# Performance work log

Hardware: AMD Instinct MI355X
Metric: run time of the kernel (lower is better)

Reference implementation:

```python
import jax, jax.numpy as jnp
import numpy as np

B, S, H = 2, 2048, 2048
NH, KVH, HD = 16, 4, 128
R = 16
LORA_SCALE = 32.0 / 16.0  # lora_alpha / lora_r
ATTN_SCALE = HD ** -0.5
NEG = -1e9


def setup_inputs() -> dict:
    key = jax.random.key(0)
    ks = jax.random.split(key, 16)
    q_dim, kv_dim = NH * HD, KVH * HD
    # RoPE tables
    inv_freq = 1.0 / (10000.0 ** (jnp.arange(0, HD, 2, dtype=jnp.float32) / HD))
    ang = jnp.arange(S, dtype=jnp.float32)[:, None] * inv_freq[None, :]  # [S, HD/2]
    emb = jnp.concatenate([ang, ang], axis=-1)  # [S, HD]
    cos = jnp.broadcast_to(jnp.cos(emb)[None], (B, S, HD))
    sin = jnp.broadcast_to(jnp.sin(emb)[None], (B, S, HD))
    # additive causal mask [B,1,S,S]
    causal = jnp.triu(jnp.full((S, S), NEG, dtype=jnp.float32), k=1)
    attention_mask = jnp.broadcast_to(causal[None, None], (B, 1, S, S))
    return {
        'hidden_states': jax.random.normal(ks[0], (B, S, H), jnp.float32),
        'cos': cos,
        'sin': sin,
        'attention_mask': attention_mask,
        'q_w': jax.random.normal(ks[1], (q_dim, H), jnp.float32) * 0.02,
        'k_w': jax.random.normal(ks[2], (kv_dim, H), jnp.float32) * 0.02,
        'v_w': jax.random.normal(ks[3], (kv_dim, H), jnp.float32) * 0.02,
        'q_b': jax.random.normal(ks[4], (q_dim,), jnp.float32) * 0.02,
        'k_b': jax.random.normal(ks[5], (kv_dim,), jnp.float32) * 0.02,
        'v_b': jax.random.normal(ks[6], (kv_dim,), jnp.float32) * 0.02,
        'q_A': jax.random.normal(ks[7], (H, R), jnp.float32) * (1.0 / np.sqrt(H)),
        'q_B': jax.random.normal(ks[8], (R, q_dim), jnp.float32) * 0.02,
        'k_A': jax.random.normal(ks[9], (H, R), jnp.float32) * (1.0 / np.sqrt(H)),
        'k_B': jax.random.normal(ks[10], (R, kv_dim), jnp.float32) * 0.02,
        'v_A': jax.random.normal(ks[11], (H, R), jnp.float32) * (1.0 / np.sqrt(H)),
        'v_B': jax.random.normal(ks[12], (R, kv_dim), jnp.float32) * 0.02,
        'o_w': jax.random.normal(ks[13], (H, H), jnp.float32) * 0.02,
    }


def _rotate_half(x):
    x1, x2 = x[..., : HD // 2], x[..., HD // 2:]
    return jnp.concatenate([-x2, x1], axis=-1)


def reference(hidden_states, cos, sin, attention_mask,
              q_w, k_w, v_w, q_b, k_b, v_b,
              q_A, q_B, k_A, k_B, v_A, v_B, o_w):
    x = hidden_states  # dropout p=0 (eval)
    # fused base + LoRA projections
    q = x @ q_w.T + q_b + LORA_SCALE * ((x @ q_A) @ q_B)  # [B,S,NH*HD]
    k = x @ k_w.T + k_b + LORA_SCALE * ((x @ k_A) @ k_B)  # [B,S,KVH*HD]
    v = x @ v_w.T + v_b + LORA_SCALE * ((x @ v_A) @ v_B)
    q = q.reshape(B, S, NH, HD).transpose(0, 2, 1, 3)   # [B,NH,S,HD]
    k = k.reshape(B, S, KVH, HD).transpose(0, 2, 1, 3)  # [B,KVH,S,HD]
    v = v.reshape(B, S, KVH, HD).transpose(0, 2, 1, 3)
    # RoPE
    c = cos[:, None]  # [B,1,S,HD]
    s = sin[:, None]
    q = q * c + _rotate_half(q) * s
    k = k * c + _rotate_half(k) * s
    # GQA: repeat kv heads
    n_rep = NH // KVH
    k = jnp.repeat(k, n_rep, axis=1)  # [B,NH,S,HD]
    v = jnp.repeat(v, n_rep, axis=1)
    scores = jnp.einsum('bhqd,bhkd->bhqk', q, k) * ATTN_SCALE
    scores = scores + attention_mask
    attn = jax.nn.softmax(scores.astype(jnp.float32), axis=-1).astype(q.dtype)
    out = jnp.einsum('bhqk,bhkd->bhqd', attn, v)
    out = out.transpose(0, 2, 1, 3).reshape(B, S, NH * HD)  # [B,S,H]
    return out @ o_w.T
```

## Files before the change

kernel.cpp:

```cpp
#include <hip/hip_runtime.h>

constexpr int cB   = 2;
constexpr int cS   = 2048;
constexpr int cH   = 2048;
constexpr int cNH  = 16;
constexpr int cKVH = 4;
constexpr int cHD  = 128;
constexpr int cQD  = 2048;
constexpr int cKVD = 512;
constexpr int cNQKV = 3072;
constexpr int cNTOK = 4096;
#define ATTN_SCALE 0.08838834764831845f
#define QSCALE 0.12751589549581288f

typedef __bf16 bf16;
typedef __attribute__((ext_vector_type(8))) __bf16 bf16x8;
typedef __attribute__((ext_vector_type(4))) __bf16 bf16x4;
typedef __attribute__((ext_vector_type(4))) float  f32x4;

__device__ __forceinline__ void async_load16(const bf16* g, bf16* l) {
    __builtin_amdgcn_global_load_lds(
        (const __attribute__((address_space(1))) void*)g,
        (__attribute__((address_space(3))) void*)l, 16, 0, 0);
}

__global__ void conv_f32_bf16(const float* __restrict__ in, bf16* __restrict__ out) {
    int i = (blockIdx.x * 256 + threadIdx.x) * 4;
    f32x4 v = *(const f32x4*)(in + i);
    bf16x4 o;
    o[0] = (bf16)v[0]; o[1] = (bf16)v[1]; o[2] = (bf16)v[2]; o[3] = (bf16)v[3];
    *(bf16x4*)(out + i) = o;
}

__global__ __launch_bounds__(256) void prep_w2(
        const float* __restrict__ qw, const float* __restrict__ kw, const float* __restrict__ vw,
        const float* __restrict__ qA, const float* __restrict__ qB,
        const float* __restrict__ kA, const float* __restrict__ kB,
        const float* __restrict__ vA, const float* __restrict__ vB,
        const float* __restrict__ qb, const float* __restrict__ kbias, const float* __restrict__ vb,
        bf16* __restrict__ Wc, float* __restrict__ biasc) {
    const int wave = threadIdx.x >> 6, lane = threadIdx.x & 63;
    const int n = blockIdx.y * 4 + wave;
    const int k0 = blockIdx.x * 512 + lane * 8;
    const float* W; const float* Am; const float* Bm; const float* bias; int nn, nd;
    if (n < cQD)             { W = qw; Am = qA; Bm = qB; bias = qb;    nn = n;               nd = cQD; }
    else if (n < cQD + cKVD) { W = kw; Am = kA; Bm = kB; bias = kbias; nn = n - cQD;         nd = cKVD; }
    else                     { W = vw; Am = vA; Bm = vB; bias = vb;    nn = n - cQD - cKVD;  nd = cKVD; }
    if (blockIdx.x == 0 && lane == 0) biasc[n] = bias[nn];
    float bm[16];
    #pragma unroll
    for (int r = 0; r < 16; ++r) bm[r] = Bm[r * nd + nn];
    const float* wrow = W + (size_t)nn * cH + k0;
    f32x4 w0 = *(const f32x4*)(wrow);
    f32x4 w1 = *(const f32x4*)(wrow + 4);
    bf16x8 o;
    #pragma unroll
    for (int j = 0; j < 8; ++j) {
        const f32x4* am = (const f32x4*)(Am + (size_t)(k0 + j) * 16);
        f32x4 a0 = am[0], a1 = am[1], a2 = am[2], a3 = am[3];
        float acc = 0.f;
        #pragma unroll
        for (int c = 0; c < 4; ++c) acc += a0[c] * bm[c] + a1[c] * bm[4 + c]
                                         + a2[c] * bm[8 + c] + a3[c] * bm[12 + c];
        const float wv = (j < 4) ? w0[j] : w1[j - 4];
        o[j] = (bf16)(wv + 2.0f * acc);
    }
    *(bf16x8*)&Wc[(size_t)n * cH + k0] = o;
}

__global__ __launch_bounds__(256) void gemm_qkv(const bf16* __restrict__ A, const bf16* __restrict__ Bw,
                                                const float* __restrict__ bias,
                                                const float* __restrict__ cosb, const float* __restrict__ sinb,
                                                bf16* __restrict__ Qr, bf16* __restrict__ Kr,
                                                bf16* __restrict__ Vt) {
    __shared__ bf16 Al[128 * 64];
    __shared__ bf16 Bl[128 * 64];
    const int tid = threadIdx.x;
    const int wave = tid >> 6, lane = tid & 63;
    const int quad = lane >> 4, l16 = lane & 15;
    const int wr = wave >> 1, wc = wave & 1;
    const long bm = (long)blockIdx.y * 128, bn = (long)blockIdx.x * 128;
    const int K = cH;

    f32x4 acc[4][4];
    #pragma unroll
    for (int i = 0; i < 4; ++i)
        #pragma unroll
        for (int c = 0; c < 4; ++c) acc[i][c] = f32x4{0.f, 0.f, 0.f, 0.f};

    int ago[4], slo[4];
    #pragma unroll
    for (int i2 = 0; i2 < 4; ++i2) {
        const int si = i2 * 256 + tid;
        const int row = si >> 3, c8 = si & 7;
        const int csw = c8 ^ (row & 7);
        ago[i2] = row * K + csw * 8;
        slo[i2] = si * 8;
    }
    const size_t bmK = (size_t)bm * K, bnK = (size_t)bn * K;
    const int sw = l16 & 7;

    for (int k0 = 0; k0 < K; k0 += 64) {
        __syncthreads();
        #pragma unroll
        for (int i2 = 0; i2 < 4; ++i2) async_load16(A  + bmK + k0 + ago[i2], Al + slo[i2]);
        #pragma unroll
        for (int i2 = 0; i2 < 4; ++i2) async_load16(Bw + bnK + k0 + ago[i2], Bl + slo[i2]);
        __syncthreads();
        #pragma unroll
        for (int ks = 0; ks < 2; ++ks) {
            const int g = ks * 4 + quad;
            const int cofs = (g ^ sw) * 8;
            bf16x8 af[4], bfr[4];
            #pragma unroll
            for (int i = 0; i < 4; ++i)
                af[i] = *(const bf16x8*)&Al[(wr * 64 + i * 16 + l16) * 64 + cofs];
            #pragma unroll
            for (int c = 0; c < 4; ++c) {
                const int nrow = wc * 32 + (c & 1) * 16 + (c >> 1) * 64 + l16;
                bfr[c] = *(const bf16x8*)&Bl[nrow * 64 + cofs];
            }
            #pragma unroll
            for (int i = 0; i < 4; ++i)
                #pragma unroll
                for (int c = 0; c < 4; ++c)
                    acc[i][c] = __builtin_amdgcn_mfma_f32_16x16x32_bf16(af[i], bfr[c], acc[i][c], 0, 0, 0);
        }
    }

    #pragma unroll
    for (int c = 0; c < 4; ++c) {
        const int nloc = wc * 32 + (c & 1) * 16 + (c >> 1) * 64 + l16;
        const float bv = bias[bn + nloc];
        #pragma unroll
        for (int i = 0; i < 4; ++i)
            #pragma unroll
            for (int r = 0; r < 4; ++r) acc[i][c][r] += bv;
    }

    const int head = (int)(bn >> 7);
    if (head < cNH + cKVH) {
        const bool isQ = head < cNH;
        #pragma unroll
        for (int cl = 0; cl < 2; ++cl) {
            const int d = wc * 32 + cl * 16 + l16;
            #pragma unroll
            for (int i = 0; i < 4; ++i)
                #pragma unroll
                for (int r = 0; r < 4; ++r) {
                    const long t = bm + wr * 64 + i * 16 + quad * 4 + r;
                    const float cv = cosb[t * cHD + d];
                    const float sv = sinb[t * cHD + d];
                    const float v1 = acc[i][cl][r], v2 = acc[i][cl + 2][r];
                    float o1 = v1 * cv - v2 * sv;
                    float o2 = v2 * cv + v1 * sv;
                    if (isQ) { o1 *= QSCALE; o2 *= QSCALE; }
                    const int b = (int)(t >> 11), s = (int)(t & 2047);
                    bf16* dst = isQ
                        ? Qr + ((size_t)(b * cNH + head) * cS + s) * cHD
                        : Kr + ((size_t)(b * cKVH + (head - cNH)) * cS + s) * cHD;
                    dst[d]      = (bf16)o1;
                    dst[d + 64] = (bf16)o2;
                }
        }
    } else {
        const int kv = head - cNH - cKVH;
        const int b = (int)(bm >> 11);
        const int sbase = (int)(bm & 2047);
        #pragma unroll
        for (int c = 0; c < 4; ++c) {
            const int d = wc * 32 + (c & 1) * 16 + (c >> 1) * 64 + l16;
            #pragma unroll
            for (int i = 0; i < 4; ++i) {
                const int s0 = sbase + wr * 64 + i * 16 + quad * 4;
                bf16x4 o4;
                #pragma unroll
                for (int r = 0; r < 4; ++r) o4[r] = (bf16)acc[i][c][r];
                *(bf16x4*)&Vt[((size_t)((b * cKVH + kv) * cHD) + d) * cS + s0] = o4;
            }
        }
    }
}

__global__ __launch_bounds__(256) void gemm_bt_f32(const bf16* __restrict__ A, const bf16* __restrict__ Bw,
                                                   float* __restrict__ Cp, int M, int N, int K) {
    __shared__ bf16 Al[128 * 64];
    __shared__ bf16 Bl[128 * 64];
    const int tid = threadIdx.x;
    const int wave = tid >> 6, lane = tid & 63;
    const int quad = lane >> 4, l16 = lane & 15;
    const int wr = wave >> 1, wc = wave & 1;
    const long bm = (long)blockIdx.y * 128, bn = (long)blockIdx.x * 128;

    f32x4 acc[4][4];
    #pragma unroll
    for (int i = 0; i < 4; ++i)
        #pragma unroll
        for (int c = 0; c < 4; ++c) acc[i][c] = f32x4{0.f, 0.f, 0.f, 0.f};

    int ago[4], slo[4];
    #pragma unroll
    for (int i2 = 0; i2 < 4; ++i2) {
        const int si = i2 * 256 + tid;
        const int row = si >> 3, c8 = si & 7;
        const int csw = c8 ^ (row & 7);
        ago[i2] = row * K + csw * 8;
        slo[i2] = si * 8;
    }
    const size_t bmK = (size_t)bm * K, bnK = (size_t)bn * K;
    const int sw = l16 & 7;

    for (int k0 = 0; k0 < K; k0 += 64) {
        __syncthreads();
        #pragma unroll
        for (int i2 = 0; i2 < 4; ++i2) async_load16(A  + bmK + k0 + ago[i2], Al + slo[i2]);
        #pragma unroll
        for (int i2 = 0; i2 < 4; ++i2) async_load16(Bw + bnK + k0 + ago[i2], Bl + slo[i2]);
        __syncthreads();
        #pragma unroll
        for (int ks = 0; ks < 2; ++ks) {
            const int cofs = ((ks * 4 + quad) ^ sw) * 8;
            bf16x8 af[4], bfr[4];
            #pragma unroll
            for (int i = 0; i < 4; ++i)
                af[i] = *(const bf16x8*)&Al[(wr * 64 + i * 16 + l16) * 64 + cofs];
            #pragma unroll
            for (int c = 0; c < 4; ++c)
                bfr[c] = *(const bf16x8*)&Bl[(wc * 64 + c * 16 + l16) * 64 + cofs];
            #pragma unroll
            for (int i = 0; i < 4; ++i)
                #pragma unroll
                for (int c = 0; c < 4; ++c)
                    acc[i][c] = __builtin_amdgcn_mfma_f32_16x16x32_bf16(af[i], bfr[c], acc[i][c], 0, 0, 0);
        }
    }

    #pragma unroll
    for (int i = 0; i < 4; ++i)
        #pragma unroll
        for (int c = 0; c < 4; ++c) {
            const long m0 = bm + wr * 64 + i * 16 + quad * 4;
            const long n  = bn + wc * 64 + c * 16 + l16;
            #pragma unroll
            for (int r = 0; r < 4; ++r)
                Cp[(m0 + r) * N + n] = acc[i][c][r];
        }
}

__global__ __launch_bounds__(256, 2) void flash4(const bf16* __restrict__ Q, const bf16* __restrict__ K,
                                                 const bf16* __restrict__ Vt, bf16* __restrict__ Ob) {
    __shared__ bf16 kb[8192];
    __shared__ bf16 vb[8192];
    __shared__ bf16 pb[4096];
    const int tid = threadIdx.x;
    const int wave = tid >> 6, lane = tid & 63;
    const int quad = lane >> 4, l16 = lane & 15;
    const int pi = blockIdx.x;
    const int h = blockIdx.y, b = blockIdx.z;

    const bf16* Qh = Q  + (size_t)(b * cNH + h) * cS * cHD;
    const bf16* Kg = K  + (size_t)(b * cKVH + (h >> 2)) * cS * cHD;
    const bf16* Vg = Vt + (size_t)(b * cKVH + (h >> 2)) * cHD * cS;

    int kgo[4], vgo[4], slo[4];
    #pragma unroll
    for (int i2 = 0; i2 < 4; ++i2) {
        const int si = i2 * 256 + tid;
        const int krow = si >> 4, kcsw = si & 15;
        const int kc = (kcsw & 8) | ((kcsw & 7) ^ (krow & 7));
        kgo[i2] = krow * cHD + kc * 8;
        const int vrow = si >> 3, vcsw = si & 7;
        const int vc = vcsw ^ (vrow & 7);
        vgo[i2] = vrow * cS + vc * 8;
        slo[i2] = si * 8;
    }

    #pragma unroll
    for (int t2 = 0; t2 < 2; ++t2) {
        const int qt = t2 == 0 ? (31 - pi) : pi;

        const bf16* Qg = Qh + (size_t)qt * 64 * cHD;
        bf16x8 qf[4];
        #pragma unroll
        for (int ks = 0; ks < 4; ++ks)
            qf[ks] = *(const bf16x8*)(Qg + (size_t)(wave * 16 + l16) * cHD + ks * 32 + quad * 8);

        f32x4 oac[8];
        #pragma unroll
        for (int dt = 0; dt < 8; ++dt) oac[dt] = f32x4{0.f, 0.f, 0.f, 0.f};
        float m_ = -3.0e38f, l_ = 0.f;

        const int nkt = qt + 1;
        for (int kt = 0; kt < nkt; ++kt) {
            __syncthreads();
            const bf16* Kt  = Kg + (size_t)kt * 64 * cHD;
            const bf16* Vtt = Vg + kt * 64;
            #pragma unroll
            for (int i2 = 0; i2 < 4; ++i2) async_load16(Kt + kgo[i2], kb + slo[i2]);
            #pragma unroll
            for (int i2 = 0; i2 < 4; ++i2) async_load16(Vtt + vgo[i2], vb + slo[i2]);
            __syncthreads();

            f32x4 st[4];
            #pragma unroll
            for (int mt = 0; mt < 4; ++mt) {
                bf16x8 kf[4];
                #pragma unroll
                for (int ks = 0; ks < 4; ++ks) {
                    const int c = ks * 4 + quad;
                    const int csw = (c & 8) | ((c & 7) ^ (l16 & 7));
                    kf[ks] = *(const bf16x8*)&kb[(mt * 16 + l16) * 128 + csw * 8];
                }
                f32x4 a = f32x4{0.f, 0.f, 0.f, 0.f};
                #pragma unroll
                for (int ks = 0; ks < 4; ++ks)
                    a = __builtin_amdgcn_mfma_f32_16x16x32_bf16(kf[ks], qf[ks], a, 0, 0, 0);
                st[mt] = a;
            }

            const int qpos = qt * 64 + wave * 16 + l16;
            float tmax = -3.0e38f;
            if ((kt * 64 + 63) > (qt * 64 + wave * 16)) {
                #pragma unroll
                for (int mt = 0; mt < 4; ++mt)
                    #pragma unroll
                    for (int r = 0; r < 4; ++r) {
                        const int kpos = kt * 64 + mt * 16 + quad * 4 + r;
                        if (kpos > qpos) st[mt][r] = -3.0e38f;
                        tmax = fmaxf(tmax, st[mt][r]);
                    }
            } else {
                #pragma unroll
                for (int mt = 0; mt < 4; ++mt)
                    #pragma unroll
                    for (int r = 0; r < 4; ++r) tmax = fmaxf(tmax, st[mt][r]);
            }
            tmax = fmaxf(tmax, __shfl_xor(tmax, 16, 64));
            tmax = fmaxf(tmax, __shfl_xor(tmax, 32, 64));
            const float mnew = fmaxf(m_, tmax);
            if (__any(tmax > m_)) {
                const float alpha = __builtin_amdgcn_exp2f(m_ - mnew);
                l_ *= alpha;
                #pragma unroll
                for (int dt = 0; dt < 8; ++dt)
                    #pragma unroll
                    for (int r = 0; r < 4; ++r) oac[dt][r] *= alpha;
            }
            m_ = mnew;
            float rs = 0.f;
            #pragma unroll
            for (int mt = 0; mt < 4; ++mt)
                #pragma unroll
                for (int r = 0; r < 4; ++r) {
                    const float p = __builtin_amdgcn_exp2f(st[mt][r] - mnew);
                    st[mt][r] = p;
                    rs += p;
                }
            rs += __shfl_xor(rs, 16, 64);
            rs += __shfl_xor(rs, 32, 64);
            l_ += rs;

            #pragma unroll
            for (int mt = 0; mt < 4; ++mt) {
                bf16x4 p4;
                #pragma unroll
                for (int r = 0; r < 4; ++r) p4[r] = (bf16)st[mt][r];
                const int csw = (mt * 2 + (quad >> 1)) ^ (l16 & 7);
                *(bf16x4*)&pb[wave * 1024 + l16 * 64 + csw * 8 + (quad & 1) * 4] = p4;
            }

            bf16x8 pf[2];
            #pragma unroll
            for (int ks = 0; ks < 2; ++ks) {
                const int c = ks * 4 + quad;
                const int csw = c ^ (l16 & 7);
                pf[ks] = *(const bf16x8*)&pb[wave * 1024 + l16 * 64 + csw * 8];
            }
            #pragma unroll
            for (int dt = 0; dt < 8; ++dt) {
                bf16x8 vf[2];
                #pragma unroll
                for (int ks = 0; ks < 2; ++ks) {
                    const int c = ks * 4 + quad;
                    const int csw = c ^ (l16 & 7);
                    vf[ks] = *(const bf16x8*)&vb[(dt * 16 + l16) * 64 + csw * 8];
                }
                #pragma unroll
                for (int ks = 0; ks < 2; ++ks)
                    oac[dt] = __builtin_amdgcn_mfma_f32_16x16x32_bf16(vf[ks], pf[ks], oac[dt], 0, 0, 0);
            }
        }

        const float inv = 1.0f / l_;
        const int token = qt * 64 + wave * 16 + l16;
        bf16* orow = Ob + (size_t)(b * cS + token) * (cNH * cHD) + h * cHD;
        #pragma unroll
        for (int dt = 0; dt < 8; ++dt) {
            bf16x4 o4;
            #pragma unroll
            for (int r = 0; r < 4; ++r) o4[r] = (bf16)(oac[dt][r] * inv);
            *(bf16x4*)&orow[dt * 16 + quad * 4] = o4;
        }
    }
}

extern "C" void kernel_launch(void* const* d_in, const int* in_sizes, int n_in,
                              void* d_out, int out_size, void* d_ws, size_t ws_size,
                              hipStream_t stream) {
    const float* x    = (const float*)d_in[0];
    const float* cosb = (const float*)d_in[1];
    const float* sinb = (const float*)d_in[2];
    const float* qw = (const float*)d_in[4];
    const float* kw = (const float*)d_in[5];
    const float* vw = (const float*)d_in[6];
    const float* qb = (const float*)d_in[7];
    const float* kb_ = (const float*)d_in[8];
    const float* vb = (const float*)d_in[9];
    const float* qA = (const float*)d_in[10];
    const float* qB = (const float*)d_in[11];
    const float* kA = (const float*)d_in[12];
    const float* kB = (const float*)d_in[13];
    const float* vA = (const float*)d_in[14];
    const float* vB = (const float*)d_in[15];
    const float* ow = (const float*)d_in[16];
    float* out = (float*)d_out;

    char* ws = (char*)d_ws;
    bf16* Xbf   = (bf16*)ws;  ws += (size_t)cNTOK * cH * 2;
    bf16* Wc    = (bf16*)ws;  ws += (size_t)cNQKV * cH * 2;
    float* biasc = (float*)ws; ws += (size_t)cNQKV * 4;
    bf16* Qr    = (bf16*)ws;  ws += (size_t)cB * cNH * cS * cHD * 2;
    bf16* Kr    = (bf16*)ws;  ws += (size_t)cB * cKVH * cS * cHD * 2;
    bf16* Vt    = (bf16*)ws;  ws += (size_t)cB * cKVH * cHD * cS * 2;
    bf16* OWbf  = (bf16*)ws;  ws += (size_t)cH * cH * 2;
    bf16* Aout  = (bf16*)ws;  ws += (size_t)cNTOK * cQD * 2;

    conv_f32_bf16<<<(cNTOK * cH) / 1024, 256, 0, stream>>>(x, Xbf);
    conv_f32_bf16<<<(cH * cH) / 1024, 256, 0, stream>>>(ow, OWbf);
    prep_w2<<<dim3(cH / 512, cNQKV / 4), 256, 0, stream>>>(qw, kw, vw, qA, qB, kA, kB, vA, vB,
                                                           qb, kb_, vb, Wc, biasc);

    gemm_qkv<<<dim3(cNQKV / 128, cNTOK / 128), 256, 0, stream>>>(Xbf, Wc, biasc, cosb, sinb, Qr, Kr, Vt);

    flash4<<<dim3(16, cNH, cB), 256, 0, stream>>>(Qr, Kr, Vt, Aout);

    gemm_bt_f32<<<dim3(cH / 128, cNTOK / 128), 256, 0, stream>>>(Aout, OWbf, out, cNTOK, cH, cH);
}
```

Measured before the change: 393.8 us.

## Double-buffer QKV and output GEMMs with larger tiles and swizzled block order

Both projection GEMMs move from 128x128 single-buffered tiles with 256 threads to 512-thread blocks with larger tiles (256x256 for QKV, 256x128 for the output projection). Global-to-LDS async loads are double-buffered and waited on with explicit vmcnt counts, so the next tile loads while the current one is multiplied. Workgroup IDs are remapped for cache locality, and s_setprio is raised around the MFMA bursts. The aim is to hide global-load latency and reuse more data per block. In exchange it uses much more LDS and more registers per thread, and the grid has fewer blocks, which may hurt occupancy or load balance.

Result: no change. 393.7 us (-0.0%).

```diff
diff --git a/kernel.cpp b/kernel.cpp
--- a/kernel.cpp
+++ b/kernel.cpp
@@ -68,94 +68,127 @@
     *(bf16x8*)&Wc[(size_t)n * cH + k0] = o;
 }
 
-__global__ __launch_bounds__(256) void gemm_qkv(const bf16* __restrict__ A, const bf16* __restrict__ Bw,
-                                                const float* __restrict__ bias,
-                                                const float* __restrict__ cosb, const float* __restrict__ sinb,
-                                                bf16* __restrict__ Qr, bf16* __restrict__ Kr,
-                                                bf16* __restrict__ Vt) {
-    __shared__ bf16 Al[128 * 64];
-    __shared__ bf16 Bl[128 * 64];
+__global__ __launch_bounds__(512, 2) void gemm_qkv2(const bf16* __restrict__ A, const bf16* __restrict__ Bw,
+                                                    const float* __restrict__ bias,
+                                                    const float* __restrict__ cosb, const float* __restrict__ sinb,
+                                                    bf16* __restrict__ Qr, bf16* __restrict__ Kr,
+                                                    bf16* __restrict__ Vt) {
+    __shared__ bf16 Al[2][256 * 64];
+    __shared__ bf16 Bl[2][256 * 64];
     const int tid = threadIdx.x;
     const int wave = tid >> 6, lane = tid & 63;
     const int quad = lane >> 4, l16 = lane & 15;
-    const int wr = wave >> 1, wc = wave & 1;
-    const long bm = (long)blockIdx.y * 128, bn = (long)blockIdx.x * 128;
+    const int wm = wave >> 2, wn = wave & 3;
     const int K = cH;
-
-    f32x4 acc[4][4];
-    #pragma unroll
-    for (int i = 0; i < 4; ++i)
-        #pragma unroll
-        for (int c = 0; c < 4; ++c) acc[i][c] = f32x4{0.f, 0.f, 0.f, 0.f};
+    constexpr int GX = cNQKV / 256;
+    constexpr int NWG = GX * (cNTOK / 256);
+
+    const int orig = blockIdx.y * GX + blockIdx.x;
+    const int swz = (orig & 7) * (NWG >> 3) + (orig >> 3);
+    const long bm = (long)(swz / GX) * 256;
+    const long bn = (long)(swz % GX) * 256;
+
+    f32x4 acc[8][4];
+    #pragma unroll
+    for (int i = 0; i < 8; ++i)
+        #pragma unroll
+        for (int j = 0; j < 4; ++j) acc[i][j] = f32x4{0.f, 0.f, 0.f, 0.f};
 
     int ago[4], slo[4];
     #pragma unroll
     for (int i2 = 0; i2 < 4; ++i2) {
-        const int si = i2 * 256 + tid;
+        const int si = i2 * 512 + tid;
         const int row = si >> 3, c8 = si & 7;
-        const int csw = c8 ^ (row & 7);
-        ago[i2] = row * K + csw * 8;
+        ago[i2] = row * K + (c8 ^ (row & 7)) * 8;
         slo[i2] = si * 8;
     }
     const size_t bmK = (size_t)bm * K, bnK = (size_t)bn * K;
+
+    auto STAGE = [&](int tt, int bb) {
+        const bf16* As_ = A  + bmK + (size_t)tt * 64;
+        const bf16* Bs_ = Bw + bnK + (size_t)tt * 64;
+        #pragma unroll
+        for (int i2 = 0; i2 < 4; ++i2) {
+            async_load16(As_ + ago[i2], &Al[bb][slo[i2]]);
+            async_load16(Bs_ + ago[i2], &Bl[bb][slo[i2]]);
+        }
+    };
+
+    constexpr int NT = cH / 64;
+    STAGE(0, 0);
+    STAGE(1, 1);
     const int sw = l16 & 7;
-
-    for (int k0 = 0; k0 < K; k0 += 64) {
-        __syncthreads();
-        #pragma unroll
-        for (int i2 = 0; i2 < 4; ++i2) async_load16(A  + bmK + k0 + ago[i2], Al + slo[i2]);
-        #pragma unroll
-        for (int i2 = 0; i2 < 4; ++i2) async_load16(Bw + bnK + k0 + ago[i2], Bl + slo[i2]);
-        __syncthreads();
-        #pragma unroll
-        for (int ks = 0; ks < 2; ++ks) {
-            const int g = ks * 4 + quad;
-            const int cofs = (g ^ sw) * 8;
-            bf16x8 af[4], bfr[4];
-            #pragma unroll
-            for (int i = 0; i < 4; ++i)
-                af[i] = *(const bf16x8*)&Al[(wr * 64 + i * 16 + l16) * 64 + cofs];
-            #pragma unroll
-            for (int c = 0; c < 4; ++c) {
-                const int nrow = wc * 32 + (c & 1) * 16 + (c >> 1) * 64 + l16;
-                bfr[c] = *(const bf16x8*)&Bl[nrow * 64 + cofs];
-            }
-            #pragma unroll
-            for (int i = 0; i < 4; ++i)
-                #pragma unroll
-                for (int c = 0; c < 4; ++c)
-                    acc[i][c] = __builtin_amdgcn_mfma_f32_16x16x32_bf16(af[i], bfr[c], acc[i][c], 0, 0, 0);
-        }
-    }
-
-    #pragma unroll
-    for (int c = 0; c < 4; ++c) {
-        const int nloc = wc * 32 + (c & 1) * 16 + (c >> 1) * 64 + l16;
+    const int arow = wm * 128 + l16;
+    const int brow = (wn >> 1) * 128 + (wn & 1) * 32 + l16;
+
+    for (int t = 0; t < NT; ++t) {
+        const int buf = t & 1;
+        if (t + 1 < NT) asm volatile("s_waitcnt vmcnt(8)" ::: "memory");
+        else            asm volatile("s_waitcnt vmcnt(0)" ::: "memory");
+        __builtin_amdgcn_s_barrier();
+        const bf16* Ab = &Al[buf][0];
+        const bf16* Bb = &Bl[buf][0];
+        #pragma unroll
+        for (int ih = 0; ih < 2; ++ih) {
+            bf16x8 af[4][2];
+            #pragma unroll
+            for (int ii = 0; ii < 4; ++ii)
+                #pragma unroll
+                for (int ks = 0; ks < 2; ++ks)
+                    af[ii][ks] = *(const bf16x8*)&Ab[(arow + (ih * 4 + ii) * 16) * 64 + (((ks * 4 + quad) ^ sw) * 8)];
+            #pragma unroll
+            for (int jh = 0; jh < 2; ++jh) {
+                bf16x8 bfr[2][2];
+                #pragma unroll
+                for (int jj = 0; jj < 2; ++jj)
+                    #pragma unroll
+                    for (int ks = 0; ks < 2; ++ks)
+                        bfr[jj][ks] = *(const bf16x8*)&Bb[(brow + jj * 16 + jh * 64) * 64 + (((ks * 4 + quad) ^ sw) * 8)];
+                __builtin_amdgcn_s_setprio(1);
+                #pragma unroll
+                for (int ii = 0; ii < 4; ++ii)
+                    #pragma unroll
+                    for (int jj = 0; jj < 2; ++jj)
+                        #pragma unroll
+                        for (int ks = 0; ks < 2; ++ks)
+                            acc[ih * 4 + ii][jh * 2 + jj] = __builtin_amdgcn_mfma_f32_16x16x32_bf16(
+                                af[ii][ks], bfr[jj][ks], acc[ih * 4 + ii][jh * 2 + jj], 0, 0, 0);
+                __builtin_amdgcn_s_setprio(0);
+            }
+        }
+        asm volatile("s_waitcnt lgkmcnt(0)" ::: "memory");
+        __builtin_amdgcn_s_barrier();
+        if (t + 2 < NT) STAGE(t + 2, buf);
+    }
+
+    #pragma unroll
+    for (int j = 0; j < 4; ++j) {
+        const int nloc = (wn >> 1) * 128 + (wn & 1) * 32 + (j & 1) * 16 + (j >> 1) * 64 + l16;
         const float bv = bias[bn + nloc];
         #pragma unroll
-        for (int i = 0; i < 4; ++i)
-            #pragma unroll
-            for (int r = 0; r < 4; ++r) acc[i][c][r] += bv;
-    }
-
-    const int head = (int)(bn >> 7);
+        for (int i = 0; i < 8; ++i)
+            #pragma unroll
+            for (int r = 0; r < 4; ++r) acc[i][j][r] += bv;
+    }
+
+    const int head = (int)(bn >> 7) + (wn >> 1);
     if (head < cNH + cKVH) {
         const bool isQ = head < cNH;
         #pragma unroll
-        for (int cl = 0; cl < 2; ++cl) {
-            const int d = wc * 32 + cl * 16 + l16;
-            #pragma unroll
-            for (int i = 0; i < 4; ++i)
+        for (int jlo = 0; jlo < 2; ++jlo) {
+            const int d = (wn & 1) * 32 + jlo * 16 + l16;
+            #pragma unroll
+            for (int i = 0; i < 8; ++i)
                 #pragma unroll
                 for (int r = 0; r < 4; ++r) {
-                    const long t = bm + wr * 64 + i * 16 + quad * 4 + r;
-                    const float cv = cosb[t * cHD + d];
-                    const float sv = sinb[t * cHD + d];
-                    const float v1 = acc[i][cl][r], v2 = acc[i][cl + 2][r];
+                    const long tok = bm + wm * 128 + i * 16 + quad * 4 + r;
+                    const float cv = cosb[tok * cHD + d];
+                    const float sv = sinb[tok * cHD + d];
+                    const float v1 = acc[i][jlo][r], v2 = acc[i][jlo + 2][r];
                     float o1 = v1 * cv - v2 * sv;
                     float o2 = v2 * cv + v1 * sv;
                     if (isQ) { o1 *= QSCALE; o2 *= QSCALE; }
-                    const int b = (int)(t >> 11), s = (int)(t & 2047);
+                    const int b = (int)(tok >> 11), s = (int)(tok & 2047);
                     bf16* dst = isQ
                         ? Qr + ((size_t)(b * cNH + head) * cS + s) * cHD
                         : Kr + ((size_t)(b * cKVH + (head - cNH)) * cS + s) * cHD;
@@ -168,82 +201,122 @@
         const int b = (int)(bm >> 11);
         const int sbase = (int)(bm & 2047);
         #pragma unroll
-        for (int c = 0; c < 4; ++c) {
-            const int d = wc * 32 + (c & 1) * 16 + (c >> 1) * 64 + l16;
-            #pragma unroll
-            for (int i = 0; i < 4; ++i) {
-                const int s0 = sbase + wr * 64 + i * 16 + quad * 4;
+        for (int j = 0; j < 4; ++j) {
+            const int d = (wn & 1) * 32 + (j & 1) * 16 + (j >> 1) * 64 + l16;
+            #pragma unroll
+            for (int i = 0; i < 8; ++i) {
+                const int s0 = sbase + wm * 128 + i * 16 + quad * 4;
                 bf16x4 o4;
                 #pragma unroll
-                for (int r = 0; r < 4; ++r) o4[r] = (bf16)acc[i][c][r];
+                for (int r = 0; r < 4; ++r) o4[r] = (bf16)acc[i][j][r];
                 *(bf16x4*)&Vt[((size_t)((b * cKVH + kv) * cHD) + d) * cS + s0] = o4;
             }
         }
     }
 }
 
-__global__ __launch_bounds__(256) void gemm_bt_f32(const bf16* __restrict__ A, const bf16* __restrict__ Bw,
-                                                   float* __restrict__ Cp, int M, int N, int K) {
-    __shared__ bf16 Al[128 * 64];
-    __shared__ bf16 Bl[128 * 64];
+__global__ __launch_bounds__(512, 2) void gemm_oproj(const bf16* __restrict__ A, const bf16* __restrict__ Bw,
+                                                     float* __restrict__ Cp) {
+    __shared__ bf16 Al[2][256 * 64];
+    __shared__ bf16 Bl[2][128 * 64];
     const int tid = threadIdx.x;
     const int wave = tid >> 6, lane = tid & 63;
     const int quad = lane >> 4, l16 = lane & 15;
-    const int wr = wave >> 1, wc = wave & 1;
-    const long bm = (long)blockIdx.y * 128, bn = (long)blockIdx.x * 128;
-
-    f32x4 acc[4][4];
-    #pragma unroll
-    for (int i = 0; i < 4; ++i)
-        #pragma unroll
-        for (int c = 0; c < 4; ++c) acc[i][c] = f32x4{0.f, 0.f, 0.f, 0.f};
-
-    int ago[4], slo[4];
+    const int wm = wave >> 2, wn = wave & 3;
+    constexpr int K = cH, N = cH;
+    constexpr int GX = cH / 128;
+    constexpr int NWG = GX * (cNTOK / 256);
+
+    const int orig = blockIdx.y * GX + blockIdx.x;
+    const int swz = (orig & 7) * (NWG >> 3) + (orig >> 3);
+    const long bm = (long)(swz / GX) * 256;
+    const long bn = (long)(swz % GX) * 128;
+
+    f32x4 acc[8][2];
+    #pragma unroll
+    for (int i = 0; i < 8; ++i)
+        #pragma unroll
+        for (int j = 0; j < 2; ++j) acc[i][j] = f32x4{0.f, 0.f, 0.f, 0.f};
+
+    int ago[4], aslo[4], bgo[2], bslo[2];
     #pragma unroll
     for (int i2 = 0; i2 < 4; ++i2) {
-        const int si = i2 * 256 + tid;
+        const int si = i2 * 512 + tid;
         const int row = si >> 3, c8 = si & 7;
-        const int csw = c8 ^ (row & 7);
-        ago[i2] = row * K + csw * 8;
-        slo[i2] = si * 8;
+        ago[i2] = row * K + (c8 ^ (row & 7)) * 8;
+        aslo[i2] = si * 8;
+    }
+    #pragma unroll
+    for (int i2 = 0; i2 < 2; ++i2) {
+        const int si = i2 * 512 + tid;
+        const int row = si >> 3, c8 = si & 7;
+        bgo[i2] = row * K + (c8 ^ (row & 7)) * 8;
+        bslo[i2] = si * 8;
     }
     const size_t bmK = (size_t)bm * K, bnK = (size_t)bn * K;
+
+    auto STAGE = [&](int tt, int bb) {
+        const bf16* As_ = A  + bmK + (size_t)tt * 64;
+        const bf16* Bs_ = Bw + bnK + (size_t)tt * 64;
+        #pragma unroll
+        for (int i2 = 0; i2 < 4; ++i2) async_load16(As_ + ago[i2], &Al[bb][aslo[i2]]);
+        #pragma unroll
+        for (int i2 = 0; i2 < 2; ++i2) async_load16(Bs_ + bgo[i2], &Bl[bb][bslo[i2]]);
+    };
+
+    constexpr int NT = K / 64;
+    STAGE(0, 0);
+    STAGE(1, 1);
     const int sw = l16 & 7;
-
-    for (int k0 = 0; k0 < K; k0 += 64) {
-        __syncthreads();
-        #pragma unroll
-        for (int i2 = 0; i2 < 4; ++i2) async_load16(A  + bmK + k0 + ago[i2], Al + slo[i2]);
-        #pragma unroll
-        for (int i2 = 0; i2 < 4; ++i2) async_load16(Bw + bnK + k0 + ago[i2], Bl + slo[i2]);
-        __syncthreads();
-        #pragma unroll
-        for (int ks = 0; ks < 2; ++ks) {
-            const int cofs = ((ks * 4 + quad) ^ sw) * 8;
-            bf16x8 af[4], bfr[4];
-            #pragma unroll
-            for (int i = 0; i < 4; ++i)
-                af[i] = *(const bf16x8*)&Al[(wr * 64 + i * 16 + l16) * 64 + cofs];
-            #pragma unroll
-            for (int c = 0; c < 4; ++c)
-                bfr[c] = *(const bf16x8*)&Bl[(wc * 64 + c * 16 + l16) * 64 + cofs];
-            #pragma unroll
-            for (int i = 0; i < 4; ++i)
-                #pragma unroll
-                for (int c = 0; c < 4; ++c)
-                    acc[i][c] = __builtin_amdgcn_mfma_f32_16x16x32_bf16(af[i], bfr[c], acc[i][c], 0, 0, 0);
-        }
-    }
-
-    #pragma unroll
-    for (int i = 0; i < 4; ++i)
-        #pragma unroll
-        for (int c = 0; c < 4; ++c) {
-            const long m0 = bm + wr * 64 + i * 16 + quad * 4;
-            const long n  = bn + wc * 64 + c * 16 + l16;
+    const int arow = wm * 128 + l16;
+    const int brow = wn * 32 + l16;
+
+    for (int t = 0; t < NT; ++t) {
+        const int buf = t & 1;
+        if (t + 1 < NT) asm volatile("s_waitcnt vmcnt(6)" ::: "memory");
+        else            asm volatile("s_waitcnt vmcnt(0)" ::: "memory");
+        __builtin_amdgcn_s_barrier();
+        const bf16* Ab = &Al[buf][0];
+        const bf16* Bb = &Bl[buf][0];
+        bf16x8 bfr[2][2];
+        #pragma unroll
+        for (int jj = 0; jj < 2; ++jj)
+            #pragma unroll
+            for (int ks = 0; ks < 2; ++ks)
+                bfr[jj][ks] = *(const bf16x8*)&Bb[(brow + jj * 16) * 64 + (((ks * 4 + quad) ^ sw) * 8)];
+        #pragma unroll
+        for (int ih = 0; ih < 2; ++ih) {
+            bf16x8 af[4][2];
+            #pragma unroll
+            for (int ii = 0; ii < 4; ++ii)
+                #pragma unroll
+                for (int ks = 0; ks < 2; ++ks)
+                    af[ii][ks] = *(const bf16x8*)&Ab[(arow + (ih * 4 + ii) * 16) * 64 + (((ks * 4 + quad) ^ sw) * 8)];
+            __builtin_amdgcn_s_setprio(1);
+            #pragma unroll
+            for (int ii = 0; ii < 4; ++ii)
+                #pragma unroll
+                for (int jj = 0; jj < 2; ++jj)
+                    #pragma unroll
+                    for (int ks = 0; ks < 2; ++ks)
+                        acc[ih * 4 + ii][jj] = __builtin_amdgcn_mfma_f32_16x16x32_bf16(
+                            af[ii][ks], bfr[jj][ks], acc[ih * 4 + ii][jj], 0, 0, 0);
+            __builtin_amdgcn_s_setprio(0);
+        }
+        asm volatile("s_waitcnt lgkmcnt(0)" ::: "memory");
+        __builtin_amdgcn_s_barrier();
+        if (t + 2 < NT) STAGE(t + 2, buf);
+    }
+
+    #pragma unroll
+    for (int i = 0; i < 8; ++i)
+        #pragma unroll
+        for (int j = 0; j < 2; ++j) {
+            const long m0 = bm + wm * 128 + i * 16 + quad * 4;
+            const long n  = bn + wn * 32 + j * 16 + l16;
             #pragma unroll
             for (int r = 0; r < 4; ++r)
-                Cp[(m0 + r) * N + n] = acc[i][c][r];
+                Cp[(m0 + r) * N + n] = acc[i][j][r];
         }
 }
 
@@ -440,9 +513,9 @@
     prep_w2<<<dim3(cH / 512, cNQKV / 4), 256, 0, stream>>>(qw, kw, vw, qA, qB, kA, kB, vA, vB,
                                                            qb, kb_, vb, Wc, biasc);
 
-    gemm_qkv<<<dim3(cNQKV / 128, cNTOK / 128), 256, 0, stream>>>(Xbf, Wc, biasc, cosb, sinb, Qr, Kr, Vt);
+    gemm_qkv2<<<dim3(cNQKV / 256, cNTOK / 256), 512, 0, stream>>>(Xbf, Wc, biasc, cosb, sinb, Qr, Kr, Vt);
 
     flash4<<<dim3(16, cNH, cB), 256, 0, stream>>>(Qr, Kr, Vt, Aout);
 
-    gemm_bt_f32<<<dim3(cH / 128, cNTOK / 128), 256, 0, stream>>>(Aout, OWbf, out, cNTOK, cH, cH);
-}
+    gemm_oproj<<<dim3(cH / 128, cNTOK / 256), 512, 0, stream>>>(Aout, OWbf, out);
+}
```
